# Optimization experiments

Hardware: AMD Instinct MI355X
Metric: run time of the kernel (lower is better)

The kernel has to match this reference:

```python
import jax, jax.numpy as jnp
import numpy as np

B = 16384          # batch size (positions)
NNZ_PER = 32       # active features per position (pieces on board)
F = 768            # 2 colors x 6 pieces x 64 squares
H = 512            # hidden_size


def setup_inputs() -> dict:
    key = jax.random.key(0)
    k1, k2, k3, k4, k5, k6 = jax.random.split(key, 6)
    nnz = B * NNZ_PER
    batch_row = jnp.repeat(jnp.arange(B, dtype=jnp.int64), NNZ_PER)
    stm_feat = jax.random.randint(k1, (nnz,), 0, F, dtype=jnp.int64)
    nstm_feat = jax.random.randint(k2, (nnz,), 0, F, dtype=jnp.int64)
    stm_indices = jnp.stack([batch_row, stm_feat])    # [2, nnz] COO (batch, feature)
    nstm_indices = jnp.stack([batch_row, nstm_feat])  # [2, nnz]
    stm_values = jnp.ones((nnz,), dtype=jnp.float32)   # binary features
    nstm_values = jnp.ones((nnz,), dtype=jnp.float32)
    W_ft = jax.random.normal(k3, (H, F), dtype=jnp.float32) * 0.02
    b_ft = jax.random.normal(k4, (H,), dtype=jnp.float32) * 0.02
    W_out = jax.random.normal(k5, (1, 2 * H), dtype=jnp.float32) * 0.02
    b_out = jax.random.normal(k6, (1,), dtype=jnp.float32) * 0.02
    return {
        "stm_indices": stm_indices,
        "nstm_indices": nstm_indices,
        "stm_values": stm_values,
        "nstm_values": nstm_values,
        "batch_size": B,
        "W_ft": W_ft,
        "b_ft": b_ft,
        "W_out": W_out,
        "b_out": b_out,
    }


def _to_dense(indices, values, batch_size):
    # torch.sparse_coo_tensor(...).to_dense(): duplicates are summed.
    dense = jnp.zeros((batch_size, F), dtype=jnp.float32)
    return dense.at[indices[0], indices[1]].add(values)


def reference(stm_indices, nstm_indices, stm_values, nstm_values, batch_size,
              W_ft, b_ft, W_out, b_out):
    stm_dense = _to_dense(stm_indices, stm_values, batch_size)     # [B, 768]
    nstm_dense = _to_dense(nstm_indices, nstm_values, batch_size)  # [B, 768]
    stm_hidden = stm_dense @ W_ft.T + b_ft     # [B, H]
    nstm_hidden = nstm_dense @ W_ft.T + b_ft   # [B, H]
    hidden = jnp.concatenate([stm_hidden, nstm_hidden], axis=1)  # [B, 2H]
    hidden = jnp.clip(hidden, 0.0, 1.0)
    return jax.nn.sigmoid(hidden @ W_out.T + b_out)  # [B, 1]
```

## Files before the change

### kernel.cpp

```cpp
#include <hip/hip_runtime.h>
#include <hip/hip_fp16.h>

#define B_SZ    16384
#define NNZ_PER 32
#define F_DIM   768
#define H_DIM   512

typedef unsigned int  uint32;
typedef unsigned long long uint64;
typedef unsigned char uchar;

__device__ inline uchar f32_to_e5m2(float x) {
    __half h = __float2half_rn(x);
    unsigned short hb = *(unsigned short*)&h;
    unsigned short lsb = (hb >> 8) & 1;
    hb = (unsigned short)(hb + 0x7F + lsb);
    return (uchar)(hb >> 8);
}

__global__ __launch_bounds__(256) void transpose_convert(
    const float* __restrict__ W, uchar* __restrict__ Wt8)
{
    __shared__ float tile[32][33];
    const int f0 = blockIdx.x * 32;
    const int h0 = blockIdx.y * 32;
    const int tx = threadIdx.x;
    const int ty = threadIdx.y;

#pragma unroll
    for (int i = 0; i < 32; i += 8)
        tile[ty + i][tx] = W[(h0 + ty + i) * F_DIM + f0 + tx];
    __syncthreads();
#pragma unroll
    for (int i = 0; i < 32; i += 8)
        Wt8[(size_t)(f0 + ty + i) * H_DIM + h0 + tx] = f32_to_e5m2(tile[tx][ty + i]);
}

__global__ __launch_bounds__(256, 4) void nnue_fwd(
    const int*   __restrict__ stm_idx,
    const int*   __restrict__ nstm_idx,
    const float* __restrict__ stm_val,
    const float* __restrict__ nstm_val,
    const uchar* __restrict__ Wt8,
    const float* __restrict__ b_ft,
    const float* __restrict__ W_out,
    const float* __restrict__ b_out,
    float* __restrict__ out)
{
    const int tid  = threadIdx.x;
    const int w    = tid >> 6;
    const int lane = tid & 63;
    const int half = lane >> 5;
    const int c    = lane & 31;
    const int b    = blockIdx.x * 4 + w;
    const int NNZ  = B_SZ * NNZ_PER;

    __shared__ uint64 sh[4][64];
    {
        const int base = b * NNZ_PER;
        int f; float v;
        if (lane < 32) { f = stm_idx [NNZ + base + lane];        v = stm_val [base + lane]; }
        else           { f = nstm_idx[NNZ + base + (lane - 32)]; v = nstm_val[base + (lane - 32)]; }
        __half2 vv = __float2half2_rn(v);
        sh[w][lane] = ((uint64)(*(uint32*)&vv) << 32) | (uint32)f;
    }
    __syncthreads();

    const uint32 selA = 0x01040004u;
    const uint32 selB = 0x03040204u;
    const uint32 coff = (uint32)c << 4;
    const char*  Wb   = (const char*)Wt8;

    __half2 z = __float2half2_rn(0.f);
    __half2 sa[8] = {z,z,z,z,z,z,z,z};
    __half2 na[8] = {z,z,z,z,z,z,z,z};

#define DECODE_FMA(acc, wv, vv)                                            \
    {                                                                      \
        uint32 p;                                                          \
        p = __builtin_amdgcn_perm(0u, wv.x, selA); acc[0] = __hfma2(*(__half2*)&p, vv, acc[0]); \
        p = __builtin_amdgcn_perm(0u, wv.x, selB); acc[1] = __hfma2(*(__half2*)&p, vv, acc[1]); \
        p = __builtin_amdgcn_perm(0u, wv.y, selA); acc[2] = __hfma2(*(__half2*)&p, vv, acc[2]); \
        p = __builtin_amdgcn_perm(0u, wv.y, selB); acc[3] = __hfma2(*(__half2*)&p, vv, acc[3]); \
        p = __builtin_amdgcn_perm(0u, wv.z, selA); acc[4] = __hfma2(*(__half2*)&p, vv, acc[4]); \
        p = __builtin_amdgcn_perm(0u, wv.z, selB); acc[5] = __hfma2(*(__half2*)&p, vv, acc[5]); \
        p = __builtin_amdgcn_perm(0u, wv.w, selA); acc[6] = __hfma2(*(__half2*)&p, vv, acc[6]); \
        p = __builtin_amdgcn_perm(0u, wv.w, selB); acc[7] = __hfma2(*(__half2*)&p, vv, acc[7]); \
    }

#pragma unroll 8
    for (int j = 0; j < 16; ++j) {
        uint64 e = sh[w][2 * j + half];
        uint32 f = (uint32)e;
        uint32 v2 = (uint32)(e >> 32);
        __half2 vv = *(__half2*)&v2;
        uint4 wv = *(const uint4*)(Wb + (((size_t)f) << 9) + coff);
        DECODE_FMA(sa, wv, vv);
    }
#pragma unroll 8
    for (int j = 0; j < 16; ++j) {
        uint64 e = sh[w][32 + 2 * j + half];
        uint32 f = (uint32)e;
        uint32 v2 = (uint32)(e >> 32);
        __half2 vv = *(__half2*)&v2;
        uint4 wv = *(const uint4*)(Wb + (((size_t)f) << 9) + coff);
        DECODE_FMA(na, wv, vv);
    }
#undef DECODE_FMA

    float s[16], n[16];
#pragma unroll
    for (int k = 0; k < 8; ++k) {
        int mi = *(int*)&sa[k];
        int oi = __shfl_xor(mi, 32, 64);
        __half2 o = *(__half2*)&oi;
        s[2 * k]     = __low2float(sa[k])  + __low2float(o);
        s[2 * k + 1] = __high2float(sa[k]) + __high2float(o);
        mi = *(int*)&na[k];
        oi = __shfl_xor(mi, 32, 64);
        o  = *(__half2*)&oi;
        n[2 * k]     = __low2float(na[k])  + __low2float(o);
        n[2 * k + 1] = __high2float(na[k]) + __high2float(o);
    }

    const float* bias = b_ft + c * 16;
    const float* wo   = W_out + half * H_DIM + c * 16;
    float dot = 0.f;
#pragma unroll
    for (int k = 0; k < 16; ++k) {
        float hv = half ? n[k] : s[k];
        float a  = fminf(fmaxf(hv + bias[k], 0.f), 1.f);
        dot += a * wo[k];
    }

#pragma unroll
    for (int off = 32; off > 0; off >>= 1)
        dot += __shfl_xor(dot, off, 64);

    if (lane == 0)
        out[b] = 1.f / (1.f + expf(-(dot + b_out[0])));
}

extern "C" void kernel_launch(void* const* d_in, const int* in_sizes, int n_in,
                              void* d_out, int out_size, void* d_ws, size_t ws_size,
                              hipStream_t stream) {
    const int*   stm_idx  = (const int*)  d_in[0];
    const int*   nstm_idx = (const int*)  d_in[1];
    const float* stm_val  = (const float*)d_in[2];
    const float* nstm_val = (const float*)d_in[3];
    const float* W_ft     = (const float*)d_in[5];
    const float* b_ft     = (const float*)d_in[6];
    const float* W_out    = (const float*)d_in[7];
    const float* b_out    = (const float*)d_in[8];
    float*       out      = (float*)d_out;
    uchar*       Wt8      = (uchar*)d_ws;

    dim3 tb(32, 8);
    dim3 tg(F_DIM / 32, H_DIM / 32);
    transpose_convert<<<tg, tb, 0, stream>>>(W_ft, Wt8);

    nnue_fwd<<<B_SZ / 4, 256, 0, stream>>>(stm_idx, nstm_idx, stm_val, nstm_val,
                                           Wt8, b_ft, W_out, b_out, out);
}
```

Before: 105.4 us.

## Stage hidden-dim weight slices in LDS and split work across slices

The hidden dimension is split into 8 slices of 64 columns. Each block loads its 768x64 fp8 weight slice into padded shared memory and gathers rows from LDS instead of global memory, for a chunk of 256 positions. A separate pack kernel precomputes LDS row offsets plus fp16 values, and a finalize kernel sums the per-slice partial dot products and applies the sigmoid. This trades scattered global/L2 gathers for LDS reads, at the cost of two extra kernel launches, a partials buffer round-trip, and each position's index list being re-read once per slice.

Result: faster. 102.0 us (-3.2%).

```diff
diff --git a/kernel.cpp b/kernel.cpp
--- a/kernel.cpp
+++ b/kernel.cpp
@@ -5,10 +5,17 @@
 #define NNZ_PER 32
 #define F_DIM   768
 #define H_DIM   512
+#define SLICE_H 64
+#define NSLICE  8
+#define CHUNK   256
+#define ROWB    80
 
 typedef unsigned int  uint32;
-typedef unsigned long long uint64;
 typedef unsigned char uchar;
+
+#define WT8_OFF  0u
+#define PK_OFF   393216u
+#define PART_OFF (393216u + 4194304u)
 
 __device__ inline uchar f32_to_e5m2(float x) {
     __half h = __float2half_rn(x);
@@ -31,53 +38,81 @@
     for (int i = 0; i < 32; i += 8)
         tile[ty + i][tx] = W[(h0 + ty + i) * F_DIM + f0 + tx];
     __syncthreads();
-#pragma unroll
-    for (int i = 0; i < 32; i += 8)
-        Wt8[(size_t)(f0 + ty + i) * H_DIM + h0 + tx] = f32_to_e5m2(tile[tx][ty + i]);
-}
-
-__global__ __launch_bounds__(256, 4) void nnue_fwd(
+    const int s = h0 >> 6;
+#pragma unroll
+    for (int i = 0; i < 32; i += 8) {
+        const int f = f0 + ty + i;
+        const int h = h0 + tx;
+        Wt8[(size_t)s * (F_DIM * SLICE_H) + f * SLICE_H + (h & 63)] =
+            f32_to_e5m2(tile[tx][ty + i]);
+    }
+}
+
+__global__ __launch_bounds__(256) void pack_entries(
     const int*   __restrict__ stm_idx,
     const int*   __restrict__ nstm_idx,
     const float* __restrict__ stm_val,
     const float* __restrict__ nstm_val,
-    const uchar* __restrict__ Wt8,
-    const float* __restrict__ b_ft,
-    const float* __restrict__ W_out,
-    const float* __restrict__ b_out,
-    float* __restrict__ out)
-{
-    const int tid  = threadIdx.x;
+    uint32* __restrict__ packed)
+{
+    const int e = blockIdx.x * 256 + threadIdx.x;
+    const int b = e >> 6, j = e & 63;
+    const int NNZ = B_SZ * NNZ_PER;
+    int f; float v;
+    if (j < 32) { f = stm_idx [NNZ + b * 32 + j];        v = stm_val [b * 32 + j]; }
+    else        { f = nstm_idx[NNZ + b * 32 + (j - 32)]; v = nstm_val[b * 32 + (j - 32)]; }
+    __half hv = __float2half_rn(v);
+    packed[e] = (uint32)(unsigned short)(f * ROWB) |
+                ((uint32)(*(unsigned short*)&hv) << 16);
+}
+
+__global__ __launch_bounds__(1024, 4) void nnue_main(
+    const uchar*  __restrict__ Wt8,
+    const uint32* __restrict__ packed,
+    const float*  __restrict__ b_ft,
+    const float*  __restrict__ W_out,
+    float* __restrict__ partials)
+{
+    __shared__ uchar Wl[F_DIM * ROWB];
+    const int tid   = threadIdx.x;
+    const int chunk = blockIdx.x;
+    const int s     = blockIdx.y;
+
+    {
+        const uchar* src = Wt8 + (size_t)s * (F_DIM * SLICE_H);
+#pragma unroll
+        for (int pass = 0; pass < 3; ++pass) {
+            const int o = pass * 16384 + tid * 16;
+            const int f = o >> 6, col = o & 63;
+            uint4 v = *(const uint4*)(src + o);
+            *(uint4*)(&Wl[f * ROWB + col]) = v;
+        }
+    }
+    __syncthreads();
+
     const int w    = tid >> 6;
     const int lane = tid & 63;
-    const int half = lane >> 5;
-    const int c    = lane & 31;
-    const int b    = blockIdx.x * 4 + w;
-    const int NNZ  = B_SZ * NNZ_PER;
-
-    __shared__ uint64 sh[4][64];
-    {
-        const int base = b * NNZ_PER;
-        int f; float v;
-        if (lane < 32) { f = stm_idx [NNZ + base + lane];        v = stm_val [base + lane]; }
-        else           { f = nstm_idx[NNZ + base + (lane - 32)]; v = nstm_val[base + (lane - 32)]; }
-        __half2 vv = __float2half2_rn(v);
-        sh[w][lane] = ((uint64)(*(uint32*)&vv) << 32) | (uint32)f;
-    }
-    __syncthreads();
+    const int hs   = lane & 3;
+    const int pl   = lane >> 2;
+    const int pos  = chunk * CHUNK + w * 16 + pl;
+    const int hb   = hs * 16;
+
+    const uint4* pk4 = (const uint4*)(packed + pos * 64);
 
     const uint32 selA = 0x01040004u;
     const uint32 selB = 0x03040204u;
-    const uint32 coff = (uint32)c << 4;
-    const char*  Wb   = (const char*)Wt8;
 
     __half2 z = __float2half2_rn(0.f);
     __half2 sa[8] = {z,z,z,z,z,z,z,z};
     __half2 na[8] = {z,z,z,z,z,z,z,z};
 
-#define DECODE_FMA(acc, wv, vv)                                            \
-    {                                                                      \
-        uint32 p;                                                          \
+#define PROC1(acc, e)                                                         \
+    {                                                                         \
+        const uint32 off = (e & 0xFFFFu) + (uint32)hb;                        \
+        uint32 vvb = __builtin_amdgcn_perm(e, e, 0x03020302u);                \
+        __half2 vv = *(__half2*)&vvb;                                         \
+        uint4 wv = *(const uint4*)(&Wl[off]);                                 \
+        uint32 p;                                                             \
         p = __builtin_amdgcn_perm(0u, wv.x, selA); acc[0] = __hfma2(*(__half2*)&p, vv, acc[0]); \
         p = __builtin_amdgcn_perm(0u, wv.x, selB); acc[1] = __hfma2(*(__half2*)&p, vv, acc[1]); \
         p = __builtin_amdgcn_perm(0u, wv.y, selA); acc[2] = __hfma2(*(__half2*)&p, vv, acc[2]); \
@@ -88,57 +123,50 @@
         p = __builtin_amdgcn_perm(0u, wv.w, selB); acc[7] = __hfma2(*(__half2*)&p, vv, acc[7]); \
     }
 
-#pragma unroll 8
-    for (int j = 0; j < 16; ++j) {
-        uint64 e = sh[w][2 * j + half];
-        uint32 f = (uint32)e;
-        uint32 v2 = (uint32)(e >> 32);
-        __half2 vv = *(__half2*)&v2;
-        uint4 wv = *(const uint4*)(Wb + (((size_t)f) << 9) + coff);
-        DECODE_FMA(sa, wv, vv);
-    }
-#pragma unroll 8
-    for (int j = 0; j < 16; ++j) {
-        uint64 e = sh[w][32 + 2 * j + half];
-        uint32 f = (uint32)e;
-        uint32 v2 = (uint32)(e >> 32);
-        __half2 vv = *(__half2*)&v2;
-        uint4 wv = *(const uint4*)(Wb + (((size_t)f) << 9) + coff);
-        DECODE_FMA(na, wv, vv);
-    }
-#undef DECODE_FMA
-
-    float s[16], n[16];
-#pragma unroll
-    for (int k = 0; k < 8; ++k) {
-        int mi = *(int*)&sa[k];
-        int oi = __shfl_xor(mi, 32, 64);
-        __half2 o = *(__half2*)&oi;
-        s[2 * k]     = __low2float(sa[k])  + __low2float(o);
-        s[2 * k + 1] = __high2float(sa[k]) + __high2float(o);
-        mi = *(int*)&na[k];
-        oi = __shfl_xor(mi, 32, 64);
-        o  = *(__half2*)&oi;
-        n[2 * k]     = __low2float(na[k])  + __low2float(o);
-        n[2 * k + 1] = __high2float(na[k]) + __high2float(o);
-    }
-
-    const float* bias = b_ft + c * 16;
-    const float* wo   = W_out + half * H_DIM + c * 16;
+    uint4 pc = pk4[0];
+#pragma unroll
+    for (int jg = 0; jg < 8; ++jg) {
+        uint4 cur = pc;
+        pc = pk4[jg + 1];
+        PROC1(sa, cur.x); PROC1(sa, cur.y); PROC1(sa, cur.z); PROC1(sa, cur.w);
+    }
+#pragma unroll
+    for (int jg = 8; jg < 16; ++jg) {
+        uint4 cur = pc;
+        if (jg < 15) pc = pk4[jg + 1];
+        PROC1(na, cur.x); PROC1(na, cur.y); PROC1(na, cur.z); PROC1(na, cur.w);
+    }
+#undef PROC1
+
+    const int h0 = s * SLICE_H + hb;
     float dot = 0.f;
 #pragma unroll
-    for (int k = 0; k < 16; ++k) {
-        float hv = half ? n[k] : s[k];
-        float a  = fminf(fmaxf(hv + bias[k], 0.f), 1.f);
-        dot += a * wo[k];
-    }
-
-#pragma unroll
-    for (int off = 32; off > 0; off >>= 1)
-        dot += __shfl_xor(dot, off, 64);
-
-    if (lane == 0)
-        out[b] = 1.f / (1.f + expf(-(dot + b_out[0])));
+    for (int i = 0; i < 8; ++i) {
+        float2 bi  = *(const float2*)(b_ft  + h0 + 2 * i);
+        float2 wsv = *(const float2*)(W_out + h0 + 2 * i);
+        float2 wnv = *(const float2*)(W_out + H_DIM + h0 + 2 * i);
+        float a0 = fminf(fmaxf(__low2float (sa[i]) + bi.x, 0.f), 1.f);
+        float a1 = fminf(fmaxf(__high2float(sa[i]) + bi.y, 0.f), 1.f);
+        float c0 = fminf(fmaxf(__low2float (na[i]) + bi.x, 0.f), 1.f);
+        float c1 = fminf(fmaxf(__high2float(na[i]) + bi.y, 0.f), 1.f);
+        dot += a0 * wsv.x + a1 * wsv.y + c0 * wnv.x + c1 * wnv.y;
+    }
+    dot += __shfl_xor(dot, 1, 64);
+    dot += __shfl_xor(dot, 2, 64);
+    if (hs == 0) partials[s * B_SZ + pos] = dot;
+}
+
+__global__ __launch_bounds__(256) void finalize(
+    const float* __restrict__ partials,
+    const float* __restrict__ b_out,
+    float* __restrict__ out)
+{
+    const int b = blockIdx.x * 256 + threadIdx.x;
+    float a = b_out[0];
+#pragma unroll
+    for (int s = 0; s < NSLICE; ++s)
+        a += partials[s * B_SZ + b];
+    out[b] = 1.f / (1.f + expf(-a));
 }
 
 extern "C" void kernel_launch(void* const* d_in, const int* in_sizes, int n_in,
@@ -153,12 +181,20 @@
     const float* W_out    = (const float*)d_in[7];
     const float* b_out    = (const float*)d_in[8];
     float*       out      = (float*)d_out;
-    uchar*       Wt8      = (uchar*)d_ws;
+
+    uchar*  Wt8      = (uchar*) ((char*)d_ws + WT8_OFF);
+    uint32* packed   = (uint32*)((char*)d_ws + PK_OFF);
+    float*  partials = (float*) ((char*)d_ws + PART_OFF);
 
     dim3 tb(32, 8);
     dim3 tg(F_DIM / 32, H_DIM / 32);
     transpose_convert<<<tg, tb, 0, stream>>>(W_ft, Wt8);
 
-    nnue_fwd<<<B_SZ / 4, 256, 0, stream>>>(stm_idx, nstm_idx, stm_val, nstm_val,
-                                           Wt8, b_ft, W_out, b_out, out);
-}
+    pack_entries<<<(B_SZ * 64) / 256, 256, 0, stream>>>(
+        stm_idx, nstm_idx, stm_val, nstm_val, packed);
+
+    dim3 grid(B_SZ / CHUNK, NSLICE);
+    nnue_main<<<grid, 1024, 0, stream>>>(Wt8, packed, b_ft, W_out, partials);
+
+    finalize<<<B_SZ / 256, 256, 0, stream>>>(partials, b_out, out);
+}
```
